# Performance work log

Measured on AMD Instinct MI355X. Metric: run time of the kernel, lower is better.

The kernel has to match this reference:

```python
import jax, jax.numpy as jnp
import numpy as np

TOP_K = 2

def setup_inputs() -> dict:
    key = jax.random.key(0)
    ks = jax.random.split(key, 5)
    N, D, E, H, O = 2048, 1024, 16, 2048, 1024
    s_in = 1.0 / np.sqrt(D)
    s_h = 1.0 / np.sqrt(H)
    return {
        "z": jax.random.normal(ks[0], (N, D), dtype=jnp.float32),
        "router_w": jax.random.normal(ks[1], (E, D), dtype=jnp.float32) * s_in,
        "router_b": jnp.zeros((E,), dtype=jnp.float32),
        "w1": jax.random.normal(ks[2], (E, H, D), dtype=jnp.float32) * s_in,
        "b1": jnp.zeros((E, H), dtype=jnp.float32),
        "w2": jax.random.normal(ks[3], (E, O, H), dtype=jnp.float32) * s_h,
        "b2": jnp.zeros((E, O), dtype=jnp.float32),
    }

def reference(z, router_w, router_b, w1, b1, w2, b2):
    # Router: softmax over experts, then top-k with renormalized weights
    logits = z @ router_w.T + router_b                      # [N, E]
    probs = jax.nn.softmax(logits, axis=-1)                 # [N, E]
    topk_prob, topk_idx = jax.lax.top_k(probs, TOP_K)       # [N, K]
    topk_prob = topk_prob / topk_prob.sum(axis=-1, keepdims=True)

    # Dense all-expert MLP (faithful to original mix(): every expert on every token)
    h = jax.nn.gelu(jnp.einsum('nd,ehd->neh', z, w1) + b1, approximate=False)  # [N, E, H]
    expert_out = jnp.einsum('neh,eoh->neo', h, w2) + b2                        # [N, E, O]

    # Gather top-k expert outputs and combine with routing weights
    picked = jnp.take_along_axis(expert_out, topk_idx[:, :, None], axis=1)     # [N, K, O]
    return (picked * topk_prob[:, :, None]).sum(axis=1)                        # [N, O]
```

## Files before the change

### kernel.cpp

```cpp
#include <hip/hip_runtime.h>
#include <hip/hip_bf16.h>
#include <math.h>

#define N_TOK 2048
#define DIM   1024
#define NE    16
#define NH    2048
#define NO    1024

typedef __attribute__((ext_vector_type(8))) short short8;
typedef __attribute__((ext_vector_type(4))) float f32x4;

__device__ __forceinline__ unsigned short f2bf(float f) {
  union { float f; unsigned u; } v; v.f = f;
  unsigned r = v.u + 0x7FFFu + ((v.u >> 16) & 1u);
  return (unsigned short)(r >> 16);
}

__device__ __forceinline__ short8 pack8(float4 a, float4 b) {
  short8 r;
  r[0] = (short)f2bf(a.x); r[1] = (short)f2bf(a.y);
  r[2] = (short)f2bf(a.z); r[3] = (short)f2bf(a.w);
  r[4] = (short)f2bf(b.x); r[5] = (short)f2bf(b.y);
  r[6] = (short)f2bf(b.z); r[7] = (short)f2bf(b.w);
  return r;
}

__device__ __forceinline__ void lds_barrier() {
  __builtin_amdgcn_s_waitcnt(0xC07F);
  __builtin_amdgcn_s_barrier();
}

__global__ __launch_bounds__(256) void router_kernel(
    const float* __restrict__ z, const float* __restrict__ rw,
    const float* __restrict__ rb, int* __restrict__ counts,
    int* __restrict__ list, float* __restrict__ tkw) {
  const int n = blockIdx.x;
  const int t = threadIdx.x;
  const int e = t >> 4, sub = t & 15;
  const float* zr = z + (size_t)n * DIM;
  const float* wr = rw + (size_t)e * DIM;
  double acc = 0.0;
#pragma unroll
  for (int i = 0; i < 16; ++i) {
    const int d = i * 64 + sub * 4;
    const float4 zv = *(const float4*)(zr + d);
    const float4 wv = *(const float4*)(wr + d);
    acc += (double)zv.x * wv.x + (double)zv.y * wv.y
         + (double)zv.z * wv.z + (double)zv.w * wv.w;
  }
  acc += __shfl_xor(acc, 8, 16);
  acc += __shfl_xor(acc, 4, 16);
  acc += __shfl_xor(acc, 2, 16);
  acc += __shfl_xor(acc, 1, 16);
  __shared__ double logits[NE];
  if (sub == 0) logits[e] = acc + (double)rb[e];
  __syncthreads();
  if (t == 0) {
    int i0 = -1, i1 = -1; double v0 = -1e300, v1 = -1e300;
    for (int i = 0; i < NE; ++i) {
      const double v = logits[i];
      if (v > v0) { v1 = v0; i1 = i0; v0 = v; i0 = i; }
      else if (v > v1) { v1 = v; i1 = i; }
    }
    const double w0 = 1.0 / (1.0 + exp(v1 - v0));
    tkw[n * 2 + 0] = (float)w0;
    tkw[n * 2 + 1] = (float)(1.0 - w0);
    const int p0 = atomicAdd(&counts[i0], 1); list[i0 * N_TOK + p0] = n * 2;
    const int p1 = atomicAdd(&counts[i1], 1); list[i1 * N_TOK + p1] = n * 2 + 1;
  }
}

#define BM 128
#define BN 64
#define BK 64
#define LDK 72
#define NNT1 (NH / BN)
#define NNT2 (NO / BN)

__device__ __forceinline__ void decode_bid(int bid, int nent, int& mt, int& ent) {
  if (bid < 2 * nent) {
    mt = (bid >> 3) & 1;
    ent = (bid >> 4) * 8 + (bid & 7);
  } else {
    const int t2 = bid - 2 * nent;
    mt = 2 + t2 / nent;
    ent = t2 - (mt - 2) * nent;
  }
}

__global__ __launch_bounds__(256, 4) void gemm1_kernel(
    const float* __restrict__ z, const float* __restrict__ w1,
    const float* __restrict__ b1, const int* __restrict__ counts,
    const int* __restrict__ list, unsigned short* __restrict__ h) {
  int mt, ent;
  decode_bid(blockIdx.x, NE * NNT1, mt, ent);
  const int e  = ent >> 5;
  const int nt = ent & 31;
  const int ne = counts[e];
  if (mt * BM >= ne) return;
  const int t = threadIdx.x;

  __shared__ unsigned short As[BM][LDK];
  __shared__ unsigned short Bs[BN][LDK];
  __shared__ int ent_s[BM];
  if (t < BM) {
    const int idx = mt * BM + t;
    ent_s[t] = (idx < ne) ? list[e * N_TOK + idx] : -1;
  }
  __syncthreads();

  const int lane = t & 63, wave = t >> 6;
  const int wm = (wave & 1) * 64, wn = (wave >> 1) * 32;
  const int l15 = lane & 15, q8 = (lane >> 4) * 8;

  f32x4 acc[4][2];
#pragma unroll
  for (int i = 0; i < 4; ++i)
#pragma unroll
    for (int j = 0; j < 2; ++j) acc[i][j] = (f32x4){0.f, 0.f, 0.f, 0.f};

  const int row8 = t >> 3;
  const int col8 = (t & 7) * 8;

  const float* aR[4];
  const float* bR[2];
  const float* bbase = w1 + ((size_t)e * NH + (size_t)nt * BN) * DIM;
#pragma unroll
  for (int p = 0; p < 4; ++p) {
    const int en = ent_s[row8 + p * 32];
    aR[p] = z + (size_t)(en >= 0 ? (en >> 1) : 0) * DIM + col8;
  }
#pragma unroll
  for (int p = 0; p < 2; ++p) bR[p] = bbase + (size_t)(row8 + p * 32) * DIM + col8;

  float4 va[4][2], vb[2][2];
#pragma unroll
  for (int p = 0; p < 4; ++p) { va[p][0] = *(const float4*)(aR[p]); va[p][1] = *(const float4*)(aR[p] + 4); }
#pragma unroll
  for (int p = 0; p < 2; ++p) { vb[p][0] = *(const float4*)(bR[p]); vb[p][1] = *(const float4*)(bR[p] + 4); }

  for (int k0 = 0; k0 < DIM; k0 += BK) {
#pragma unroll
    for (int p = 0; p < 4; ++p)
      *(short8*)&As[row8 + p * 32][col8] = pack8(va[p][0], va[p][1]);
#pragma unroll
    for (int p = 0; p < 2; ++p)
      *(short8*)&Bs[row8 + p * 32][col8] = pack8(vb[p][0], vb[p][1]);
    lds_barrier();
    if (k0 + BK < DIM) {
      const int kn = k0 + BK;
#pragma unroll
      for (int p = 0; p < 4; ++p) { va[p][0] = *(const float4*)(aR[p] + kn); va[p][1] = *(const float4*)(aR[p] + kn + 4); }
#pragma unroll
      for (int p = 0; p < 2; ++p) { vb[p][0] = *(const float4*)(bR[p] + kn); vb[p][1] = *(const float4*)(bR[p] + kn + 4); }
    }
#pragma unroll
    for (int kk = 0; kk < BK; kk += 32) {
      short8 a[4], b[2];
#pragma unroll
      for (int i = 0; i < 4; ++i) a[i] = *(const short8*)&As[wm + i * 16 + l15][kk + q8];
#pragma unroll
      for (int j = 0; j < 2; ++j) b[j] = *(const short8*)&Bs[wn + j * 16 + l15][kk + q8];
#pragma unroll
      for (int i = 0; i < 4; ++i)
#pragma unroll
        for (int j = 0; j < 2; ++j)
          acc[i][j] = __builtin_amdgcn_mfma_f32_16x16x32_bf16(a[i], b[j], acc[i][j], 0, 0, 0);
    }
    lds_barrier();
  }

  const int r4 = (lane >> 4) * 4;
#pragma unroll
  for (int i = 0; i < 4; ++i) {
#pragma unroll
    for (int reg = 0; reg < 4; ++reg) {
      const int row = wm + i * 16 + r4 + reg;
      const int en = ent_s[row];
      if (en < 0) continue;
      unsigned short* hrow = h + (size_t)en * NH;
#pragma unroll
      for (int j = 0; j < 2; ++j) {
        const int col = nt * BN + wn + j * 16 + l15;
        float v = acc[i][j][reg] + b1[e * NH + col];
        v = 0.5f * v * (1.0f + erff(v * 0.70710678118654752f));
        hrow[col] = f2bf(v);
      }
    }
  }
}

__global__ __launch_bounds__(256, 4) void gemm2_kernel(
    const unsigned short* __restrict__ h, const float* __restrict__ w2,
    const float* __restrict__ b2, const int* __restrict__ counts,
    const int* __restrict__ list, float* __restrict__ contrib) {
  int mt, ent;
  decode_bid(blockIdx.x, NE * NNT2, mt, ent);
  const int e  = ent >> 4;
  const int nt = ent & 15;
  const int ne = counts[e];
  if (mt * BM >= ne) return;
  const int t = threadIdx.x;

  __shared__ unsigned short As[BM][LDK];
  __shared__ unsigned short Bs[BN][LDK];
  __shared__ int ent_s[BM];
  if (t < BM) {
    const int idx = mt * BM + t;
    ent_s[t] = (idx < ne) ? list[e * N_TOK + idx] : -1;
  }
  __syncthreads();

  const int lane = t & 63, wave = t >> 6;
  const int wm = (wave & 1) * 64, wn = (wave >> 1) * 32;
  const int l15 = lane & 15, q8 = (lane >> 4) * 8;

  f32x4 acc[4][2];
#pragma unroll
  for (int i = 0; i < 4; ++i)
#pragma unroll
    for (int j = 0; j < 2; ++j) acc[i][j] = (f32x4){0.f, 0.f, 0.f, 0.f};

  const int row8 = t >> 3;
  const int col8 = (t & 7) * 8;

  const unsigned short* aR[4];
#pragma unroll
  for (int p = 0; p < 4; ++p) {
    const int en = ent_s[row8 + p * 32];
    aR[p] = h + (size_t)(en >= 0 ? en : 0) * NH + col8;
  }
  const float* bR[2];
  const float* bbase = w2 + ((size_t)e * NO + (size_t)nt * BN) * NH;
#pragma unroll
  for (int p = 0; p < 2; ++p) bR[p] = bbase + (size_t)(row8 + p * 32) * NH + col8;

  float4 va[4], vb[2][2];
#pragma unroll
  for (int p = 0; p < 4; ++p) va[p] = *(const float4*)(aR[p]);
#pragma unroll
  for (int p = 0; p < 2; ++p) { vb[p][0] = *(const float4*)(bR[p]); vb[p][1] = *(const float4*)(bR[p] + 4); }

  for (int k0 = 0; k0 < NH; k0 += BK) {
#pragma unroll
    for (int p = 0; p < 4; ++p)
      *(float4*)&As[row8 + p * 32][col8] = va[p];
#pragma unroll
    for (int p = 0; p < 2; ++p)
      *(short8*)&Bs[row8 + p * 32][col8] = pack8(vb[p][0], vb[p][1]);
    lds_barrier();
    if (k0 + BK < NH) {
      const int kn = k0 + BK;
#pragma unroll
      for (int p = 0; p < 4; ++p) va[p] = *(const float4*)(aR[p] + kn);
#pragma unroll
      for (int p = 0; p < 2; ++p) { vb[p][0] = *(const float4*)(bR[p] + kn); vb[p][1] = *(const float4*)(bR[p] + kn + 4); }
    }
#pragma unroll
    for (int kk = 0; kk < BK; kk += 32) {
      short8 a[4], b[2];
#pragma unroll
      for (int i = 0; i < 4; ++i) a[i] = *(const short8*)&As[wm + i * 16 + l15][kk + q8];
#pragma unroll
      for (int j = 0; j < 2; ++j) b[j] = *(const short8*)&Bs[wn + j * 16 + l15][kk + q8];
#pragma unroll
      for (int i = 0; i < 4; ++i)
#pragma unroll
        for (int j = 0; j < 2; ++j)
          acc[i][j] = __builtin_amdgcn_mfma_f32_16x16x32_bf16(a[i], b[j], acc[i][j], 0, 0, 0);
    }
    lds_barrier();
  }

  const int r4 = (lane >> 4) * 4;
#pragma unroll
  for (int i = 0; i < 4; ++i) {
#pragma unroll
    for (int reg = 0; reg < 4; ++reg) {
      const int row = wm + i * 16 + r4 + reg;
      const int en = ent_s[row];
      if (en < 0) continue;
      float* crow = contrib + (size_t)en * NO;
#pragma unroll
      for (int j = 0; j < 2; ++j) {
        const int col = nt * BN + wn + j * 16 + l15;
        crow[col] = acc[i][j][reg] + b2[e * NO + col];
      }
    }
  }
}

__global__ __launch_bounds__(256) void combine_kernel(
    const float* __restrict__ contrib, const float* __restrict__ tkw,
    float* __restrict__ out) {
  const int gid = blockIdx.x * 256 + threadIdx.x;
  const int n = gid >> 8;
  const int c = (gid & 255) * 4;
  const float w0 = tkw[n * 2], w1 = tkw[n * 2 + 1];
  const float4 a = *(const float4*)(contrib + (size_t)(n * 2) * NO + c);
  const float4 b = *(const float4*)(contrib + (size_t)(n * 2 + 1) * NO + c);
  float4 o;
  o.x = w0 * a.x + w1 * b.x; o.y = w0 * a.y + w1 * b.y;
  o.z = w0 * a.z + w1 * b.z; o.w = w0 * a.w + w1 * b.w;
  *(float4*)(out + (size_t)n * NO + c) = o;
}

extern "C" void kernel_launch(void* const* d_in, const int* in_sizes, int n_in,
                              void* d_out, int out_size, void* d_ws, size_t ws_size,
                              hipStream_t stream) {
  const float* z  = (const float*)d_in[0];
  const float* rw = (const float*)d_in[1];
  const float* rb = (const float*)d_in[2];
  const float* w1 = (const float*)d_in[3];
  const float* b1 = (const float*)d_in[4];
  const float* w2 = (const float*)d_in[5];
  const float* b2 = (const float*)d_in[6];
  float* out = (float*)d_out;

  char* ws = (char*)d_ws;
  int*   counts = (int*)ws;
  int*   list   = (int*)(ws + 256);
  float* tkw    = (float*)(ws + 256 + 131072);
  unsigned short* h = (unsigned short*)(ws + 262144);
  float* contrib = (float*)(ws + 262144 + 16777216);

  hipMemsetAsync(counts, 0, NE * sizeof(int), stream);
  router_kernel<<<N_TOK, 256, 0, stream>>>(z, rw, rb, counts, list, tkw);
  gemm1_kernel<<<16 * NE * NNT1, 256, 0, stream>>>(z, w1, b1, counts, list, h);
  gemm2_kernel<<<16 * NE * NNT2, 256, 0, stream>>>(h, w2, b2, counts, list, contrib);
  combine_kernel<<<(N_TOK * (NO / 4)) / 256, 256, 0, stream>>>(contrib, tkw, out);
}
```

Before: 497.4 us.

## Stream GEMM tiles directly into swizzled LDS with wider N tiles and bf16 z

Adds a pre-pass that converts z to bf16 once. Both expert GEMMs now load tiles straight from global memory into XOR-swizzled LDS with global_load_lds. The weight tile stays fp32 in LDS and is converted to bf16 when fragments are read. BN grows to 128, so each wave computes a 64x64 sub-tile, and occupancy drops to 2 blocks per SM. The aim is to cut register staging, duplicate A-row reloads and per-block conversion work, but the register-prefetch overlap is removed and the M-tile grid is capped at 8 levels, which assumes no expert receives more than 1024 token slots.

New measurement: 427.8 us. 1.16x faster.

```diff
diff --git a/kernel.cpp b/kernel.cpp
--- a/kernel.cpp
+++ b/kernel.cpp
@@ -24,6 +24,25 @@
   r[4] = (short)f2bf(b.x); r[5] = (short)f2bf(b.y);
   r[6] = (short)f2bf(b.z); r[7] = (short)f2bf(b.w);
   return r;
+}
+
+__device__ __forceinline__ unsigned pkbf(float x, float y) {
+  float2 f; f.x = x; f.y = y;
+  __hip_bfloat162 b = __float22bfloat162_rn(f);
+  unsigned u; __builtin_memcpy(&u, &b, 4);
+  return u;
+}
+__device__ __forceinline__ short8 cvt8(float4 a, float4 b) {
+  union { short8 s; unsigned u[4]; } r;
+  r.u[0] = pkbf(a.x, a.y); r.u[1] = pkbf(a.z, a.w);
+  r.u[2] = pkbf(b.x, b.y); r.u[3] = pkbf(b.z, b.w);
+  return r.s;
+}
+
+__device__ __forceinline__ void glds16(const void* g, void* l) {
+  __builtin_amdgcn_global_load_lds(
+      (const __attribute__((address_space(1))) void*)g,
+      (__attribute__((address_space(3))) void*)l, 16, 0, 0);
 }
 
 __device__ __forceinline__ void lds_barrier() {
@@ -71,12 +90,20 @@
   }
 }
 
+__global__ __launch_bounds__(256) void convert_z_kernel(
+    const float* __restrict__ z, unsigned short* __restrict__ zbf) {
+  const int i = (blockIdx.x * 256 + threadIdx.x) * 8;
+  const float4 a = *(const float4*)(z + i);
+  const float4 b = *(const float4*)(z + i + 4);
+  *(short8*)(zbf + i) = pack8(a, b);
+}
+
 #define BM 128
-#define BN 64
+#define BN 128
 #define BK 64
-#define LDK 72
 #define NNT1 (NH / BN)
 #define NNT2 (NO / BN)
+#define MT_LEVELS 8
 
 __device__ __forceinline__ void decode_bid(int bid, int nent, int& mt, int& ent) {
   if (bid < 2 * nent) {
@@ -89,20 +116,20 @@
   }
 }
 
-__global__ __launch_bounds__(256, 4) void gemm1_kernel(
-    const float* __restrict__ z, const float* __restrict__ w1,
+__global__ __launch_bounds__(256, 2) void gemm1_kernel(
+    const unsigned short* __restrict__ zbf, const float* __restrict__ w1,
     const float* __restrict__ b1, const int* __restrict__ counts,
     const int* __restrict__ list, unsigned short* __restrict__ h) {
   int mt, ent;
   decode_bid(blockIdx.x, NE * NNT1, mt, ent);
-  const int e  = ent >> 5;
-  const int nt = ent & 31;
+  const int e  = ent >> 4;
+  const int nt = ent & 15;
   const int ne = counts[e];
   if (mt * BM >= ne) return;
   const int t = threadIdx.x;
 
-  __shared__ unsigned short As[BM][LDK];
-  __shared__ unsigned short Bs[BN][LDK];
+  __shared__ __align__(16) unsigned char As[BM * BK * 2];
+  __shared__ __align__(16) unsigned char Bs[BN * BK * 4];
   __shared__ int ent_s[BM];
   if (t < BM) {
     const int idx = mt * BM + t;
@@ -110,68 +137,75 @@
   }
   __syncthreads();
 
-  const int lane = t & 63, wave = t >> 6;
-  const int wm = (wave & 1) * 64, wn = (wave >> 1) * 32;
-  const int l15 = lane & 15, q8 = (lane >> 4) * 8;
-
-  f32x4 acc[4][2];
+  const int lane = t & 63, w = t >> 6;
+  const unsigned short* aP[4];
+  const float* bP[8];
+  unsigned char *aL[4], *bL[8];
+  {
+    const int l3 = lane >> 3, c7 = lane & 7;
+#pragma unroll
+    for (int p = 0; p < 4; ++p) {
+      const int CI = w + 4 * p;
+      const int R = 8 * CI + l3;
+      const int c = c7 ^ (R & 7);
+      const int en = ent_s[R];
+      aP[p] = zbf + (size_t)(en >= 0 ? (en >> 1) : 0) * DIM + c * 8;
+      aL[p] = As + CI * 1024;
+    }
+    const int l4 = lane >> 4, c15 = lane & 15;
+    const float* bbase = w1 + ((size_t)e * NH + (size_t)nt * BN) * DIM;
+#pragma unroll
+    for (int q = 0; q < 8; ++q) {
+      const int CI = w + 4 * q;
+      const int R = 4 * CI + l4;
+      const int c = c15 ^ (R & 15);
+      bP[q] = bbase + (size_t)R * DIM + c * 4;
+      bL[q] = Bs + CI * 1024;
+    }
+  }
+
+  const int wm = (w & 1) * 64, wn = (w >> 1) * 64;
+  const int l15 = lane & 15, quad = lane >> 4;
+
+  f32x4 acc[4][4];
 #pragma unroll
   for (int i = 0; i < 4; ++i)
 #pragma unroll
-    for (int j = 0; j < 2; ++j) acc[i][j] = (f32x4){0.f, 0.f, 0.f, 0.f};
-
-  const int row8 = t >> 3;
-  const int col8 = (t & 7) * 8;
-
-  const float* aR[4];
-  const float* bR[2];
-  const float* bbase = w1 + ((size_t)e * NH + (size_t)nt * BN) * DIM;
-#pragma unroll
-  for (int p = 0; p < 4; ++p) {
-    const int en = ent_s[row8 + p * 32];
-    aR[p] = z + (size_t)(en >= 0 ? (en >> 1) : 0) * DIM + col8;
-  }
-#pragma unroll
-  for (int p = 0; p < 2; ++p) bR[p] = bbase + (size_t)(row8 + p * 32) * DIM + col8;
-
-  float4 va[4][2], vb[2][2];
-#pragma unroll
-  for (int p = 0; p < 4; ++p) { va[p][0] = *(const float4*)(aR[p]); va[p][1] = *(const float4*)(aR[p] + 4); }
-#pragma unroll
-  for (int p = 0; p < 2; ++p) { vb[p][0] = *(const float4*)(bR[p]); vb[p][1] = *(const float4*)(bR[p] + 4); }
+    for (int j = 0; j < 4; ++j) acc[i][j] = (f32x4){0.f, 0.f, 0.f, 0.f};
 
   for (int k0 = 0; k0 < DIM; k0 += BK) {
 #pragma unroll
-    for (int p = 0; p < 4; ++p)
-      *(short8*)&As[row8 + p * 32][col8] = pack8(va[p][0], va[p][1]);
-#pragma unroll
-    for (int p = 0; p < 2; ++p)
-      *(short8*)&Bs[row8 + p * 32][col8] = pack8(vb[p][0], vb[p][1]);
+    for (int p = 0; p < 4; ++p) glds16(aP[p] + k0, aL[p]);
+#pragma unroll
+    for (int q = 0; q < 8; ++q) glds16(bP[q] + k0, bL[q]);
+    __syncthreads();
+#pragma unroll
+    for (int kk = 0; kk < BK; kk += 32) {
+      short8 af[4], bfr[4];
+#pragma unroll
+      for (int i = 0; i < 4; ++i) {
+        const int R = wm + i * 16 + l15;
+        const int c0 = (kk >> 3) + quad;
+        af[i] = *(const short8*)(As + R * 128 + ((c0 ^ (R & 7)) << 4));
+      }
+#pragma unroll
+      for (int j = 0; j < 4; ++j) {
+        const int R = wn + j * 16 + l15;
+        const int c0 = (kk >> 2) + 2 * quad;
+        const float4 f0 = *(const float4*)(Bs + R * 256 + ((c0 ^ (R & 15)) << 4));
+        const float4 f1 = *(const float4*)(Bs + R * 256 + (((c0 + 1) ^ (R & 15)) << 4));
+        bfr[j] = cvt8(f0, f1);
+      }
+#pragma unroll
+      for (int i = 0; i < 4; ++i)
+#pragma unroll
+        for (int j = 0; j < 4; ++j)
+          acc[i][j] = __builtin_amdgcn_mfma_f32_16x16x32_bf16(af[i], bfr[j], acc[i][j], 0, 0, 0);
+    }
     lds_barrier();
-    if (k0 + BK < DIM) {
-      const int kn = k0 + BK;
-#pragma unroll
-      for (int p = 0; p < 4; ++p) { va[p][0] = *(const float4*)(aR[p] + kn); va[p][1] = *(const float4*)(aR[p] + kn + 4); }
-#pragma unroll
-      for (int p = 0; p < 2; ++p) { vb[p][0] = *(const float4*)(bR[p] + kn); vb[p][1] = *(const float4*)(bR[p] + kn + 4); }
-    }
-#pragma unroll
-    for (int kk = 0; kk < BK; kk += 32) {
-      short8 a[4], b[2];
-#pragma unroll
-      for (int i = 0; i < 4; ++i) a[i] = *(const short8*)&As[wm + i * 16 + l15][kk + q8];
-#pragma unroll
-      for (int j = 0; j < 2; ++j) b[j] = *(const short8*)&Bs[wn + j * 16 + l15][kk + q8];
-#pragma unroll
-      for (int i = 0; i < 4; ++i)
-#pragma unroll
-        for (int j = 0; j < 2; ++j)
-          acc[i][j] = __builtin_amdgcn_mfma_f32_16x16x32_bf16(a[i], b[j], acc[i][j], 0, 0, 0);
-    }
-    lds_barrier();
-  }
-
-  const int r4 = (lane >> 4) * 4;
+  }
+
+  const int r4 = quad * 4;
 #pragma unroll
   for (int i = 0; i < 4; ++i) {
 #pragma unroll
@@ -181,7 +215,7 @@
       if (en < 0) continue;
       unsigned short* hrow = h + (size_t)en * NH;
 #pragma unroll
-      for (int j = 0; j < 2; ++j) {
+      for (int j = 0; j < 4; ++j) {
         const int col = nt * BN + wn + j * 16 + l15;
         float v = acc[i][j][reg] + b1[e * NH + col];
         v = 0.5f * v * (1.0f + erff(v * 0.70710678118654752f));
@@ -191,20 +225,20 @@
   }
 }
 
-__global__ __launch_bounds__(256, 4) void gemm2_kernel(
+__global__ __launch_bounds__(256, 2) void gemm2_kernel(
     const unsigned short* __restrict__ h, const float* __restrict__ w2,
     const float* __restrict__ b2, const int* __restrict__ counts,
     const int* __restrict__ list, float* __restrict__ contrib) {
   int mt, ent;
   decode_bid(blockIdx.x, NE * NNT2, mt, ent);
-  const int e  = ent >> 4;
-  const int nt = ent & 15;
+  const int e  = ent >> 3;
+  const int nt = ent & 7;
   const int ne = counts[e];
   if (mt * BM >= ne) return;
   const int t = threadIdx.x;
 
-  __shared__ unsigned short As[BM][LDK];
-  __shared__ unsigned short Bs[BN][LDK];
+  __shared__ __align__(16) unsigned char As[BM * BK * 2];
+  __shared__ __align__(16) unsigned char Bs[BN * BK * 4];
   __shared__ int ent_s[BM];
   if (t < BM) {
     const int idx = mt * BM + t;
@@ -212,68 +246,75 @@
   }
   __syncthreads();
 
-  const int lane = t & 63, wave = t >> 6;
-  const int wm = (wave & 1) * 64, wn = (wave >> 1) * 32;
-  const int l15 = lane & 15, q8 = (lane >> 4) * 8;
-
-  f32x4 acc[4][2];
+  const int lane = t & 63, w = t >> 6;
+  const unsigned short* aP[4];
+  const float* bP[8];
+  unsigned char *aL[4], *bL[8];
+  {
+    const int l3 = lane >> 3, c7 = lane & 7;
+#pragma unroll
+    for (int p = 0; p < 4; ++p) {
+      const int CI = w + 4 * p;
+      const int R = 8 * CI + l3;
+      const int c = c7 ^ (R & 7);
+      const int en = ent_s[R];
+      aP[p] = h + (size_t)(en >= 0 ? en : 0) * NH + c * 8;
+      aL[p] = As + CI * 1024;
+    }
+    const int l4 = lane >> 4, c15 = lane & 15;
+    const float* bbase = w2 + ((size_t)e * NO + (size_t)nt * BN) * NH;
+#pragma unroll
+    for (int q = 0; q < 8; ++q) {
+      const int CI = w + 4 * q;
+      const int R = 4 * CI + l4;
+      const int c = c15 ^ (R & 15);
+      bP[q] = bbase + (size_t)R * NH + c * 4;
+      bL[q] = Bs + CI * 1024;
+    }
+  }
+
+  const int wm = (w & 1) * 64, wn = (w >> 1) * 64;
+  const int l15 = lane & 15, quad = lane >> 4;
+
+  f32x4 acc[4][4];
 #pragma unroll
   for (int i = 0; i < 4; ++i)
 #pragma unroll
-    for (int j = 0; j < 2; ++j) acc[i][j] = (f32x4){0.f, 0.f, 0.f, 0.f};
-
-  const int row8 = t >> 3;
-  const int col8 = (t & 7) * 8;
-
-  const unsigned short* aR[4];
-#pragma unroll
-  for (int p = 0; p < 4; ++p) {
-    const int en = ent_s[row8 + p * 32];
-    aR[p] = h + (size_t)(en >= 0 ? en : 0) * NH + col8;
-  }
-  const float* bR[2];
-  const float* bbase = w2 + ((size_t)e * NO + (size_t)nt * BN) * NH;
-#pragma unroll
-  for (int p = 0; p < 2; ++p) bR[p] = bbase + (size_t)(row8 + p * 32) * NH + col8;
-
-  float4 va[4], vb[2][2];
-#pragma unroll
-  for (int p = 0; p < 4; ++p) va[p] = *(const float4*)(aR[p]);
-#pragma unroll
-  for (int p = 0; p < 2; ++p) { vb[p][0] = *(const float4*)(bR[p]); vb[p][1] = *(const float4*)(bR[p] + 4); }
+    for (int j = 0; j < 4; ++j) acc[i][j] = (f32x4){0.f, 0.f, 0.f, 0.f};
 
   for (int k0 = 0; k0 < NH; k0 += BK) {
 #pragma unroll
-    for (int p = 0; p < 4; ++p)
-      *(float4*)&As[row8 + p * 32][col8] = va[p];
-#pragma unroll
-    for (int p = 0; p < 2; ++p)
-      *(short8*)&Bs[row8 + p * 32][col8] = pack8(vb[p][0], vb[p][1]);
+    for (int p = 0; p < 4; ++p) glds16(aP[p] + k0, aL[p]);
+#pragma unroll
+    for (int q = 0; q < 8; ++q) glds16(bP[q] + k0, bL[q]);
+    __syncthreads();
+#pragma unroll
+    for (int kk = 0; kk < BK; kk += 32) {
+      short8 af[4], bfr[4];
+#pragma unroll
+      for (int i = 0; i < 4; ++i) {
+        const int R = wm + i * 16 + l15;
+        const int c0 = (kk >> 3) + quad;
+        af[i] = *(const short8*)(As + R * 128 + ((c0 ^ (R & 7)) << 4));
+      }
+#pragma unroll
+      for (int j = 0; j < 4; ++j) {
+        const int R = wn + j * 16 + l15;
+        const int c0 = (kk >> 2) + 2 * quad;
+        const float4 f0 = *(const float4*)(Bs + R * 256 + ((c0 ^ (R & 15)) << 4));
+        const float4 f1 = *(const float4*)(Bs + R * 256 + (((c0 + 1) ^ (R & 15)) << 4));
+        bfr[j] = cvt8(f0, f1);
+      }
+#pragma unroll
+      for (int i = 0; i < 4; ++i)
+#pragma unroll
+        for (int j = 0; j < 4; ++j)
+          acc[i][j] = __builtin_amdgcn_mfma_f32_16x16x32_bf16(af[i], bfr[j], acc[i][j], 0, 0, 0);
+    }
     lds_barrier();
-    if (k0 + BK < NH) {
-      const int kn = k0 + BK;
-#pragma unroll
-      for (int p = 0; p < 4; ++p) va[p] = *(const float4*)(aR[p] + kn);
-#pragma unroll
-      for (int p = 0; p < 2; ++p) { vb[p][0] = *(const float4*)(bR[p] + kn); vb[p][1] = *(const float4*)(bR[p] + kn + 4); }
-    }
-#pragma unroll
-    for (int kk = 0; kk < BK; kk += 32) {
-      short8 a[4], b[2];
-#pragma unroll
-      for (int i = 0; i < 4; ++i) a[i] = *(const short8*)&As[wm + i * 16 + l15][kk + q8];
-#pragma unroll
-      for (int j = 0; j < 2; ++j) b[j] = *(const short8*)&Bs[wn + j * 16 + l15][kk + q8];
-#pragma unroll
-      for (int i = 0; i < 4; ++i)
-#pragma unroll
-        for (int j = 0; j < 2; ++j)
-          acc[i][j] = __builtin_amdgcn_mfma_f32_16x16x32_bf16(a[i], b[j], acc[i][j], 0, 0, 0);
-    }
-    lds_barrier();
-  }
-
-  const int r4 = (lane >> 4) * 4;
+  }
+
+  const int r4 = quad * 4;
 #pragma unroll
   for (int i = 0; i < 4; ++i) {
 #pragma unroll
@@ -283,7 +324,7 @@
       if (en < 0) continue;
       float* crow = contrib + (size_t)en * NO;
 #pragma unroll
-      for (int j = 0; j < 2; ++j) {
+      for (int j = 0; j < 4; ++j) {
         const int col = nt * BN + wn + j * 16 + l15;
         crow[col] = acc[i][j][reg] + b2[e * NO + col];
       }
@@ -322,12 +363,14 @@
   int*   counts = (int*)ws;
   int*   list   = (int*)(ws + 256);
   float* tkw    = (float*)(ws + 256 + 131072);
-  unsigned short* h = (unsigned short*)(ws + 262144);
-  float* contrib = (float*)(ws + 262144 + 16777216);
+  unsigned short* zbf = (unsigned short*)(ws + 262144);
+  unsigned short* h = (unsigned short*)(ws + 262144 + 4194304);
+  float* contrib = (float*)(ws + 262144 + 4194304 + 16777216);
 
   hipMemsetAsync(counts, 0, NE * sizeof(int), stream);
+  convert_z_kernel<<<(N_TOK * DIM / 8) / 256, 256, 0, stream>>>(z, zbf);
   router_kernel<<<N_TOK, 256, 0, stream>>>(z, rw, rb, counts, list, tkw);
-  gemm1_kernel<<<16 * NE * NNT1, 256, 0, stream>>>(z, w1, b1, counts, list, h);
-  gemm2_kernel<<<16 * NE * NNT2, 256, 0, stream>>>(h, w2, b2, counts, list, contrib);
+  gemm1_kernel<<<MT_LEVELS * NE * NNT1, 256, 0, stream>>>(zbf, w1, b1, counts, list, h);
+  gemm2_kernel<<<MT_LEVELS * NE * NNT2, 256, 0, stream>>>(h, w2, b2, counts, list, contrib);
   combine_kernel<<<(N_TOK * (NO / 4)) / 256, 256, 0, stream>>>(contrib, tkw, out);
 }
```
